# Kernel optimization log

Measured on AMD Instinct MI355X. Metric: run time of the kernel, lower is better.

Reference implementation:

```python
import jax, jax.numpy as jnp
import numpy as np

N = 100000   # KG_E: number of entities
D = 128      # hidden_dim == out_dim
H = 4        # n_heads
DH = D // H  # att_size
E = 1200000  # KG edges (avg degree 12)


def _layer_norm(x, g, b, eps=1e-5):
    mu = jnp.mean(x, -1, keepdims=True)
    var = jnp.mean((x - mu) ** 2, -1, keepdims=True)
    return (x - mu) * jax.lax.rsqrt(var + eps) * g + b


def setup_inputs() -> dict:
    key = jax.random.key(0)
    ks = jax.random.split(key, 16)
    p = lambda i, s: jax.random.normal(ks[i], s, jnp.float32) * 0.02
    loops = jnp.arange(N, dtype=jnp.int32)
    return {
        "ent_embed": jax.random.normal(ks[0], (N, D), jnp.float32),
        "edge_weight": jax.random.uniform(ks[1], (E,), jnp.float32),
        "ln1_g": jnp.ones(D, jnp.float32), "ln1_b": jnp.zeros(D, jnp.float32),
        "wq": p(2, (D, D)), "bq": jnp.zeros(D, jnp.float32),
        "wk": p(3, (D, D)), "bk": jnp.zeros(D, jnp.float32),
        "wv": p(4, (D, D)), "bv": jnp.zeros(D, jnp.float32),
        "wo": p(5, (D, D)), "bo": jnp.zeros(D, jnp.float32),
        "ln2_g": jnp.ones(D, jnp.float32), "ln2_b": jnp.zeros(D, jnp.float32),
        "w1": p(6, (D, D)), "b1": jnp.zeros(D, jnp.float32),  # ffn_size == hidden_dim here
        "w2": p(7, (D, D)), "b2": jnp.zeros(D, jnp.float32),
        "lmbda12": jnp.array([np.log10(6.0), 2.2 - np.log10(6.0)], jnp.float32),
        "gat_w": p(8, (D, D)), "gat_b": jnp.zeros(D, jnp.float32),
        "w_atten_r": p(9, (2 * D, 1)),
        "prelu_a": jnp.array(0.25, jnp.float32),
        "edge_index": jax.random.randint(ks[10], (2, E), 0, N, jnp.int32),
        "batch_ids": loops,
        # drop_neigh(drop_prob=0): batch COO edges + appended self-loops (node_num -> batch_ids)
        "batch_edge_index": jnp.concatenate(
            [jax.random.randint(ks[11], (2, E), 0, N, jnp.int32),
             jnp.stack([loops, loops])], axis=1),
    }


def _forward(ent_embed, edge_weight, ln1_g, ln1_b, wq, bq, wk, bk, wv, bv, wo, bo,
             ln2_g, ln2_b, w1, b1, w2, b2, lmbda12, gat_w, gat_b, w_atten_r, prelu_a,
             edge_index, batch_ids, batch_edge_index):
    # ---- pre-LN transformer encoder block; each entity is a length-1 sequence ----
    y = _layer_norm(ent_embed, ln1_g, ln1_b)
    q = (y @ wq + bq).reshape(N, H, DH)
    k = (y @ wk + bk).reshape(N, H, DH)
    v = (y @ wv + bv).reshape(N, H, DH)
    logits = jnp.sum(q * (DH ** -0.5) * k, -1, keepdims=True)  # [N,H,1]: single kv position
    attn = jax.nn.softmax(logits, axis=-1)                     # == 1.0 since seq_len == 1
    ctx = (attn * v).reshape(N, D)
    x = ent_embed + (ctx @ wo + bo)
    y = _layer_norm(x, ln2_g, ln2_b)
    gcn_in = x + (jax.nn.gelu(y @ w1 + b1, approximate=False) @ w2 + b2)

    # ---- GCN layer: lambda-weighted neighbor mean via sparse spmm ----
    row, col = edge_index[0], edge_index[1]
    neigh_sum = jax.ops.segment_sum(edge_weight[:, None] * gcn_in[col], row, num_segments=N)
    rowsum = jax.ops.segment_sum(edge_weight, row, num_segments=N)[:, None]
    l1, l2 = lmbda12[0], lmbda12[1]
    gcn_out = (gcn_in + l2 * neigh_sum) / (1.0 + l2 * rowsum) * l1

    # ---- GAT layer: gather -> per-edge attention -> scatter-normalize ----
    gat_in = gcn_out @ gat_w + gat_b
    brow, bcol = batch_edge_index[0], batch_edge_index[1]
    # cat([l, r]) @ w  ==  l @ w[:D] + r @ w[D:]  (avoids [E, 2D] intermediate)
    s_l = gat_in[batch_ids] @ w_atten_r[:D, 0]   # per left-slot node scalar
    s_r = gat_in @ w_atten_r[D:, 0]              # per node scalar
    e = s_l[brow] + s_r[bcol]
    att = jnp.exp(-jnp.where(e > 0, e, 0.2 * e))  # exp(-leaky_relu(e, 0.2))
    e_rowsum = jax.ops.segment_sum(att, brow, num_segments=N)[:, None]
    e_out = jax.ops.segment_sum(att[:, None] * gat_in[bcol], brow, num_segments=N)
    e_out = e_out * (1.0 / e_rowsum)
    return jnp.where(e_out > 0, e_out, prelu_a * e_out)  # PReLU


def reference(ent_embed, edge_weight, ln1_g, ln1_b, wq, bq, wk, bk, wv, bv, wo, bo,
              ln2_g, ln2_b, w1, b1, w2, b2, lmbda12, gat_w, gat_b, w_atten_r, prelu_a,
              edge_index, batch_ids, batch_edge_index):
    return _forward(ent_embed, edge_weight, ln1_g, ln1_b, wq, bq, wk, bk, wv, bv, wo, bo,
                    ln2_g, ln2_b, w1, b1, w2, b2, lmbda12, gat_w, gat_b, w_atten_r, prelu_a,
                    edge_index, batch_ids, batch_edge_index)
```

## Files before the change

### kernel.cpp

```cpp
#include <hip/hip_runtime.h>
#include <hip/hip_bf16.h>
#include <math.h>

#define D 128

typedef __attribute__((ext_vector_type(8))) short bf16x8_t;
typedef __attribute__((ext_vector_type(4))) float f32x4_t;

__device__ __forceinline__ unsigned short f2bf(float f){
    unsigned int x = __float_as_uint(f);
    unsigned int r = x + 0x7FFFu + ((x >> 16) & 1u);
    return (unsigned short)(r >> 16);
}

__device__ __forceinline__ float gelu_exact(float x){
    return 0.5f * x * (1.0f + erff(x * 0.70710678118654752f));
}


template<int R>
__device__ __forceinline__ void multiReduce(float* red, int j){
    __syncthreads();
    #pragma unroll
    for (int s = 64; s > 0; s >>= 1){
        if (j < s){
            #pragma unroll
            for (int r = 0; r < R; ++r) red[r*D + j] += red[r*D + j + s];
        }
        __syncthreads();
    }
}

template<int R>
__device__ __forceinline__ void matvec(const float* sh, const float* __restrict__ W,
                                       const float* __restrict__ bias, int j, float* acc){
    float bb = bias[j];
    #pragma unroll
    for (int r = 0; r < R; ++r) acc[r] = bb;
    #pragma unroll 8
    for (int i = 0; i < D; ++i){
        float w = W[i*D + j];
        #pragma unroll
        for (int r = 0; r < R; ++r) acc[r] += sh[r*D + i] * w;
    }
}

__global__ __launch_bounds__(256)
void k_cvt(const float* __restrict__ w0, const float* __restrict__ w1,
           const float* __restrict__ w2, const float* __restrict__ w3,
           unsigned short* __restrict__ out)
{
    int m = blockIdx.y;
    const float* W = (m == 0) ? w0 : (m == 1) ? w1 : (m == 2) ? w2 : w3;
    int o = blockIdx.x * 256 + threadIdx.x;
    int j  = o & 7;
    int l  = (o >> 3) & 63;
    int k0 = (o >> 9) & 3;
    int s  = o >> 11;
    int k  = 32*k0 + 8*(l >> 4) + j;
    int nn = 16*s + (l & 15);
    out[(size_t)m * 16384 + o] = f2bf(W[k*D + nn]);
}


__device__ __forceinline__ void mm_stage(const unsigned short* __restrict__ Wp,
                                         const float* __restrict__ bias,
                                         const unsigned short (*Xw)[136],
                                         int c, int g, int l, f32x4_t acc[8])
{
    #pragma unroll
    for (int s = 0; s < 8; ++s){
        float bb = bias[16*s + c];
        acc[s] = (f32x4_t){bb, bb, bb, bb};
    }
    #pragma unroll
    for (int k0 = 0; k0 < 4; ++k0){
        bf16x8_t a = *(const bf16x8_t*)&Xw[c][32*k0 + 8*g];
        #pragma unroll
        for (int s = 0; s < 8; ++s){
            bf16x8_t b = *(const bf16x8_t*)&Wp[(size_t)(((s*4 + k0)*64 + l) * 8)];
            acc[s] = __builtin_amdgcn_mfma_f32_16x16x32_bf16(a, b, acc[s], 0, 0, 0);
        }
    }
}

__global__ __launch_bounds__(256)
void k_dense(const float* __restrict__ ent,
             const float* __restrict__ g1, const float* __restrict__ be1,
             const float* __restrict__ g2, const float* __restrict__ be2,
             const float* __restrict__ bv, const float* __restrict__ bo,
             const float* __restrict__ b1, const float* __restrict__ b2,
             const unsigned short* __restrict__ Wp,
             float* __restrict__ gcn_in, int n)
{
    __shared__ unsigned short X[4][16][136];
    const int tid = threadIdx.x;
    const int wv_ = tid >> 6, l = tid & 63, c = l & 15, g = l >> 4;
    const int row0 = blockIdx.x * 64 + wv_ * 16;
    unsigned short (*Xw)[136] = X[wv_];

    float ev[8][4];
    #pragma unroll
    for (int s = 0; s < 8; ++s)
        #pragma unroll
        for (int r = 0; r < 4; ++r){
            int rr = row0 + 4*g + r; if (rr >= n) rr = n - 1;
            ev[s][r] = ent[(size_t)rr * D + 16*s + c];
        }

    {
        float gg[8], bb[8];
        #pragma unroll
        for (int s = 0; s < 8; ++s){ gg[s] = g1[16*s + c]; bb[s] = be1[16*s + c]; }
        #pragma unroll
        for (int r = 0; r < 4; ++r){
            float t = 0.0f;
            #pragma unroll
            for (int s = 0; s < 8; ++s) t += ev[s][r];
            t += __shfl_xor(t,1); t += __shfl_xor(t,2); t += __shfl_xor(t,4); t += __shfl_xor(t,8);
            float mu = t * (1.0f/128.0f);
            float q = 0.0f;
            #pragma unroll
            for (int s = 0; s < 8; ++s){ float d = ev[s][r]-mu; q += d*d; }
            q += __shfl_xor(q,1); q += __shfl_xor(q,2); q += __shfl_xor(q,4); q += __shfl_xor(q,8);
            float rs = rsqrtf(q*(1.0f/128.0f) + 1e-5f);
            #pragma unroll
            for (int s = 0; s < 8; ++s)
                Xw[4*g + r][16*s + c] = f2bf((ev[s][r]-mu)*rs*gg[s] + bb[s]);
        }
    }

    f32x4_t acc[8];

    mm_stage(Wp + 0*16384, bv, Xw, c, g, l, acc);
    #pragma unroll
    for (int s = 0; s < 8; ++s)
        #pragma unroll
        for (int r = 0; r < 4; ++r)
            Xw[4*g + r][16*s + c] = f2bf(acc[s][r]);

    mm_stage(Wp + 1*16384, bo, Xw, c, g, l, acc);
    #pragma unroll
    for (int s = 0; s < 8; ++s)
        #pragma unroll
        for (int r = 0; r < 4; ++r)
            ev[s][r] += acc[s][r];

    {
        float gg[8], bb[8];
        #pragma unroll
        for (int s = 0; s < 8; ++s){ gg[s] = g2[16*s + c]; bb[s] = be2[16*s + c]; }
        #pragma unroll
        for (int r = 0; r < 4; ++r){
            float t = 0.0f;
            #pragma unroll
            for (int s = 0; s < 8; ++s) t += ev[s][r];
            t += __shfl_xor(t,1); t += __shfl_xor(t,2); t += __shfl_xor(t,4); t += __shfl_xor(t,8);
            float mu = t * (1.0f/128.0f);
            float q = 0.0f;
            #pragma unroll
            for (int s = 0; s < 8; ++s){ float d = ev[s][r]-mu; q += d*d; }
            q += __shfl_xor(q,1); q += __shfl_xor(q,2); q += __shfl_xor(q,4); q += __shfl_xor(q,8);
            float rs = rsqrtf(q*(1.0f/128.0f) + 1e-5f);
            #pragma unroll
            for (int s = 0; s < 8; ++s)
                Xw[4*g + r][16*s + c] = f2bf((ev[s][r]-mu)*rs*gg[s] + bb[s]);
        }
    }

    mm_stage(Wp + 2*16384, b1, Xw, c, g, l, acc);
    #pragma unroll
    for (int s = 0; s < 8; ++s)
        #pragma unroll
        for (int r = 0; r < 4; ++r)
            Xw[4*g + r][16*s + c] = f2bf(gelu_exact(acc[s][r]));

    mm_stage(Wp + 3*16384, b2, Xw, c, g, l, acc);
    #pragma unroll
    for (int s = 0; s < 8; ++s)
        #pragma unroll
        for (int r = 0; r < 4; ++r){
            int rr = row0 + 4*g + r;
            if (rr < n) gcn_in[(size_t)rr * D + 16*s + c] = ev[s][r] + acc[s][r];
        }
}


__global__ __launch_bounds__(256)
void k_hist(const int* __restrict__ rows, int* __restrict__ deg, int E){
    int i = blockIdx.x * 256 + threadIdx.x;
    if (i < E) atomicAdd(&deg[rows[i]], 1);
}

__global__ __launch_bounds__(256)
void k_scan_partial(const int* __restrict__ deg, int* __restrict__ bsum, int n){
    __shared__ int s[256];
    int i = blockIdx.x * 256 + threadIdx.x;
    s[threadIdx.x] = (i < n) ? deg[i] : 0;
    __syncthreads();
    #pragma unroll
    for (int st = 128; st > 0; st >>= 1){
        if (threadIdx.x < st) s[threadIdx.x] += s[threadIdx.x + st];
        __syncthreads();
    }
    if (threadIdx.x == 0) bsum[blockIdx.x] = s[0];
}

__global__ __launch_bounds__(1024)
void k_scan_bsums(int* __restrict__ bsum, int nb){
    __shared__ int a[1024], b[1024];
    int t = threadIdx.x;
    int orig = (t < nb) ? bsum[t] : 0;
    int *src = a, *dst = b;
    src[t] = orig;
    __syncthreads();
    for (int off = 1; off < 1024; off <<= 1){
        dst[t] = src[t] + ((t >= off) ? src[t-off] : 0);
        __syncthreads();
        int* tmp = src; src = dst; dst = tmp;
    }
    if (t < nb) bsum[t] = src[t] - orig;
}

__global__ __launch_bounds__(256)
void k_scan_final(const int* __restrict__ deg, const int* __restrict__ bsum,
                  int* __restrict__ start, int* __restrict__ cur, int n, int total){
    __shared__ int a[256], b[256];
    int t = threadIdx.x;
    int i = blockIdx.x * 256 + t;
    int orig = (i < n) ? deg[i] : 0;
    int *src = a, *dst = b;
    src[t] = orig;
    __syncthreads();
    for (int off = 1; off < 256; off <<= 1){
        dst[t] = src[t] + ((t >= off) ? src[t-off] : 0);
        __syncthreads();
        int* tmp = src; src = dst; dst = tmp;
    }
    int excl = src[t] - orig + bsum[blockIdx.x];
    if (i < n){ start[i] = excl; cur[i] = excl; }
    if (i == n-1) start[n] = total;
}

__global__ __launch_bounds__(256)
void k_fill_gcn(const int* __restrict__ eidx, const float* __restrict__ ew,
                int* __restrict__ cur, int* __restrict__ colp, float* __restrict__ wp, int E){
    int i = blockIdx.x * 256 + threadIdx.x;
    if (i < E){
        int r = eidx[i];
        int pos = atomicAdd(&cur[r], 1);
        colp[pos] = eidx[E + i];
        wp[pos]   = ew[i];
    }
}

__global__ __launch_bounds__(256)
void k_fill_gat(const int* __restrict__ beidx, int* __restrict__ cur,
                int* __restrict__ colp, int E2){
    int i = blockIdx.x * 256 + threadIdx.x;
    if (i < E2){
        int r = beidx[i];
        int pos = atomicAdd(&cur[r], 1);
        colp[pos] = beidx[E2 + i];
    }
}

template<int R>
__global__ __launch_bounds__(128)
void k_gcn_pull_fin(const float* __restrict__ gcn_in,
                    const int* __restrict__ start, const int* __restrict__ colp,
                    const float* __restrict__ wp,
                    const float* __restrict__ lmbda,
                    const float* __restrict__ gat_w, const float* __restrict__ gat_b,
                    const float* __restrict__ watt,
                    float* __restrict__ gat_in,
                    float* __restrict__ dl, float* __restrict__ dr, int n)
{
    const int j = threadIdx.x;
    const int row0 = blockIdx.x * R;
    __shared__ float sh[R*D];
    __shared__ float red[R*D];
    float l1 = lmbda[0], l2 = lmbda[1];

    #pragma unroll
    for (int r = 0; r < R; ++r){
        int rr = row0 + r;
        if (rr < n){
            float acc = 0.0f, wsum = 0.0f;
            int s0 = start[rr], s1 = start[rr+1];
            for (int e = s0; e < s1; ++e){
                int   c = colp[e];
                float w = wp[e];
                acc  += w * gcn_in[(size_t)c * D + j];
                wsum += w;
            }
            float base = gcn_in[(size_t)rr * D + j];
            sh[r*D + j] = (base + l2 * acc) / (1.0f + l2 * wsum) * l1;
        } else {
            sh[r*D + j] = 0.0f;
        }
    }
    __syncthreads();

    float gv[R]; matvec<R>(sh, gat_w, gat_b, j, gv);
    #pragma unroll
    for (int r = 0; r < R; ++r){
        int rr = row0 + r;
        if (rr < n) gat_in[(size_t)rr * D + j] = gv[r];
    }

    float wl = watt[j], wr = watt[D + j];
    __syncthreads();
    #pragma unroll
    for (int r = 0; r < R; ++r) red[r*D + j] = gv[r] * wl;
    multiReduce<R>(red, j);
    if (j == 0){
        #pragma unroll
        for (int r = 0; r < R; ++r){ int rr = row0 + r; if (rr < n) dl[rr] = red[r*D]; }
    }
    __syncthreads();
    #pragma unroll
    for (int r = 0; r < R; ++r) red[r*D + j] = gv[r] * wr;
    multiReduce<R>(red, j);
    if (j == 0){
        #pragma unroll
        for (int r = 0; r < R; ++r){ int rr = row0 + r; if (rr < n) dr[rr] = red[r*D]; }
    }
}

template<int R>
__global__ __launch_bounds__(128)
void k_gat_out(const float* __restrict__ gat_in,
               const int* __restrict__ start2, const int* __restrict__ colp2,
               const int* __restrict__ bids,
               const float* __restrict__ dl, const float* __restrict__ dr,
               const float* __restrict__ prelu_a,
               float* __restrict__ out, int n)
{
    const int j = threadIdx.x;
    const int row0 = blockIdx.x * R;
    float pa = prelu_a[0];

    #pragma unroll
    for (int r = 0; r < R; ++r){
        int rr = row0 + r;
        if (rr < n){
            float dlv = dl[bids[rr]];
            int s0 = start2[rr], s1 = start2[rr+1];
            float acc = 0.0f, es = 0.0f;
            for (int e = s0; e < s1; ++e){
                int c = colp2[e];
                float ev = dlv + dr[c];
                float lr = ev > 0.0f ? ev : 0.2f * ev;
                float att = __expf(-lr);
                es  += att;
                acc += att * gat_in[(size_t)c * D + j];
            }
            float v = acc / es;
            out[(size_t)rr * D + j] = v > 0.0f ? v : pa * v;
        }
    }
}


extern "C" void kernel_launch(void* const* d_in, const int* in_sizes, int n_in,
                              void* d_out, int out_size, void* d_ws, size_t ws_size,
                              hipStream_t stream)
{
    const float* ent   = (const float*)d_in[0];
    const float* ew    = (const float*)d_in[1];
    const float* ln1_g = (const float*)d_in[2];
    const float* ln1_b = (const float*)d_in[3];
    const float* wv    = (const float*)d_in[8];
    const float* bv    = (const float*)d_in[9];
    const float* wo    = (const float*)d_in[10];
    const float* bo    = (const float*)d_in[11];
    const float* ln2_g = (const float*)d_in[12];
    const float* ln2_b = (const float*)d_in[13];
    const float* w1    = (const float*)d_in[14];
    const float* b1    = (const float*)d_in[15];
    const float* w2    = (const float*)d_in[16];
    const float* b2    = (const float*)d_in[17];
    const float* lmbda = (const float*)d_in[18];
    const float* gat_w = (const float*)d_in[19];
    const float* gat_b = (const float*)d_in[20];
    const float* watt  = (const float*)d_in[21];
    const float* prelu = (const float*)d_in[22];
    const int* eidx    = (const int*)d_in[23];
    const int* bids    = (const int*)d_in[24];
    const int* beidx   = (const int*)d_in[25];

    const int n  = in_sizes[24];
    const int E  = in_sizes[1];
    const int E2 = in_sizes[25] / 2;

    char* ws = (char*)d_ws;
    const size_t szND = (size_t)n * D * sizeof(float);
    size_t off = 0;
    float* bufA   = (float*)(ws + off); off += szND;
    float* bufB   = (float*)(ws + off); off += szND;
    float* dl     = (float*)(ws + off); off += (size_t)n * 4;
    float* dr     = (float*)(ws + off); off += (size_t)n * 4;
    int*   deg1   = (int*)(ws + off);   off += (size_t)n * 4;
    int*   deg2   = (int*)(ws + off);   off += (size_t)n * 4;
    int*   start1 = (int*)(ws + off);   off += (size_t)(n+1) * 4;
    int*   start2 = (int*)(ws + off);   off += (size_t)(n+1) * 4;
    int*   cur1   = (int*)(ws + off);   off += (size_t)n * 4;
    int*   cur2   = (int*)(ws + off);   off += (size_t)n * 4;
    int*   bsum   = (int*)(ws + off);   off += 1024 * 4;
    int*   colp1  = (int*)(ws + off);   off += (size_t)E * 4;
    float* wp1    = (float*)(ws + off); off += (size_t)E * 4;
    int*   colp2  = (int*)(ws + off);   off += (size_t)E2 * 4;
    off = (off + 15) & ~(size_t)15;
    unsigned short* Wp = (unsigned short*)(ws + off); off += (size_t)4 * 16384 * 2;

    constexpr int R = 4;
    const int nblk  = (n + R - 1) / R;
    const int nscan = (n + 255) / 256;

    k_cvt<<<dim3(64, 4), 256, 0, stream>>>(wv, wo, w1, w2, Wp);

    k_dense<<<(n + 63)/64, 256, 0, stream>>>(ent, ln1_g, ln1_b, ln2_g, ln2_b,
                                             bv, bo, b1, b2, Wp, bufA, n);

    hipMemsetAsync(deg1, 0, (size_t)2 * n * 4, stream);
    k_hist<<<(E + 255)/256, 256, 0, stream>>>(eidx, deg1, E);
    k_hist<<<(E2 + 255)/256, 256, 0, stream>>>(beidx, deg2, E2);

    k_scan_partial<<<nscan, 256, 0, stream>>>(deg1, bsum, n);
    k_scan_bsums<<<1, 1024, 0, stream>>>(bsum, nscan);
    k_scan_final<<<nscan, 256, 0, stream>>>(deg1, bsum, start1, cur1, n, E);
    k_fill_gcn<<<(E + 255)/256, 256, 0, stream>>>(eidx, ew, cur1, colp1, wp1, E);

    k_scan_partial<<<nscan, 256, 0, stream>>>(deg2, bsum, n);
    k_scan_bsums<<<1, 1024, 0, stream>>>(bsum, nscan);
    k_scan_final<<<nscan, 256, 0, stream>>>(deg2, bsum, start2, cur2, n, E2);
    k_fill_gat<<<(E2 + 255)/256, 256, 0, stream>>>(beidx, cur2, colp2, E2);

    k_gcn_pull_fin<R><<<nblk, 128, 0, stream>>>(bufA, start1, colp1, wp1, lmbda,
                                                gat_w, gat_b, watt, bufB, dl, dr, n);

    k_gat_out<R><<<nblk, 128, 0, stream>>>(bufB, start2, colp2, bids, dl, dr,
                                           prelu, (float*)d_out, n);
}
```

Baseline: 845.6 us.

## Fold GAT linear into dense kernel before aggregation; wave-per-row float2 pulls

The GAT projection (gat_w) is now applied per node inside the MFMA dense kernel, before the GCN neighbour aggregation. This relies on linearity: the weighted mean of projected rows equals the projection of the weighted mean, with the bias added afterwards. It removes the scalar fp32 matvec and the shared-memory reductions from the gather kernel. Both gather kernels now assign one wave per row, have each lane load float2, and compute dl/dr with wave shuffles. The cost is an extra bf16 rounding of the pre-projection activations, which can slightly change numerics.

Result: faster. 728.4 us (-13.9%).

```diff
diff --git a/kernel.cpp b/kernel.cpp
--- a/kernel.cpp
+++ b/kernel.cpp
@@ -17,41 +17,20 @@
     return 0.5f * x * (1.0f + erff(x * 0.70710678118654752f));
 }
 
-
-template<int R>
-__device__ __forceinline__ void multiReduce(float* red, int j){
-    __syncthreads();
-    #pragma unroll
-    for (int s = 64; s > 0; s >>= 1){
-        if (j < s){
-            #pragma unroll
-            for (int r = 0; r < R; ++r) red[r*D + j] += red[r*D + j + s];
-        }
-        __syncthreads();
-    }
-}
-
-template<int R>
-__device__ __forceinline__ void matvec(const float* sh, const float* __restrict__ W,
-                                       const float* __restrict__ bias, int j, float* acc){
-    float bb = bias[j];
-    #pragma unroll
-    for (int r = 0; r < R; ++r) acc[r] = bb;
-    #pragma unroll 8
-    for (int i = 0; i < D; ++i){
-        float w = W[i*D + j];
-        #pragma unroll
-        for (int r = 0; r < R; ++r) acc[r] += sh[r*D + i] * w;
-    }
+__device__ __forceinline__ float waveSum(float v){
+    #pragma unroll
+    for (int m = 1; m < 64; m <<= 1) v += __shfl_xor(v, m, 64);
+    return v;
 }
 
 __global__ __launch_bounds__(256)
 void k_cvt(const float* __restrict__ w0, const float* __restrict__ w1,
            const float* __restrict__ w2, const float* __restrict__ w3,
+           const float* __restrict__ w4,
            unsigned short* __restrict__ out)
 {
     int m = blockIdx.y;
-    const float* W = (m == 0) ? w0 : (m == 1) ? w1 : (m == 2) ? w2 : w3;
+    const float* W = (m == 0) ? w0 : (m == 1) ? w1 : (m == 2) ? w2 : (m == 3) ? w3 : w4;
     int o = blockIdx.x * 256 + threadIdx.x;
     int j  = o & 7;
     int l  = (o >> 3) & 63;
@@ -63,6 +42,7 @@
 }
 
 
+template<bool HASB>
 __device__ __forceinline__ void mm_stage(const unsigned short* __restrict__ Wp,
                                          const float* __restrict__ bias,
                                          const unsigned short (*Xw)[136],
@@ -70,7 +50,7 @@
 {
     #pragma unroll
     for (int s = 0; s < 8; ++s){
-        float bb = bias[16*s + c];
+        float bb = HASB ? bias[16*s + c] : 0.0f;
         acc[s] = (f32x4_t){bb, bb, bb, bb};
     }
     #pragma unroll
@@ -91,7 +71,7 @@
              const float* __restrict__ bv, const float* __restrict__ bo,
              const float* __restrict__ b1, const float* __restrict__ b2,
              const unsigned short* __restrict__ Wp,
-             float* __restrict__ gcn_in, int n)
+             float* __restrict__ Zout, int n)
 {
     __shared__ unsigned short X[4][16][136];
     const int tid = threadIdx.x;
@@ -132,14 +112,14 @@
 
     f32x4_t acc[8];
 
-    mm_stage(Wp + 0*16384, bv, Xw, c, g, l, acc);
+    mm_stage<true>(Wp + 0*16384, bv, Xw, c, g, l, acc);
     #pragma unroll
     for (int s = 0; s < 8; ++s)
         #pragma unroll
         for (int r = 0; r < 4; ++r)
             Xw[4*g + r][16*s + c] = f2bf(acc[s][r]);
 
-    mm_stage(Wp + 1*16384, bo, Xw, c, g, l, acc);
+    mm_stage<true>(Wp + 1*16384, bo, Xw, c, g, l, acc);
     #pragma unroll
     for (int s = 0; s < 8; ++s)
         #pragma unroll
@@ -168,20 +148,27 @@
         }
     }
 
-    mm_stage(Wp + 2*16384, b1, Xw, c, g, l, acc);
+    mm_stage<true>(Wp + 2*16384, b1, Xw, c, g, l, acc);
     #pragma unroll
     for (int s = 0; s < 8; ++s)
         #pragma unroll
         for (int r = 0; r < 4; ++r)
             Xw[4*g + r][16*s + c] = f2bf(gelu_exact(acc[s][r]));
 
-    mm_stage(Wp + 3*16384, b2, Xw, c, g, l, acc);
+    mm_stage<true>(Wp + 3*16384, b2, Xw, c, g, l, acc);
+    #pragma unroll
+    for (int s = 0; s < 8; ++s)
+        #pragma unroll
+        for (int r = 0; r < 4; ++r)
+            Xw[4*g + r][16*s + c] = f2bf(ev[s][r] + acc[s][r]);
+
+    mm_stage<false>(Wp + 4*16384, nullptr, Xw, c, g, l, acc);
     #pragma unroll
     for (int s = 0; s < 8; ++s)
         #pragma unroll
         for (int r = 0; r < 4; ++r){
             int rr = row0 + 4*g + r;
-            if (rr < n) gcn_in[(size_t)rr * D + 16*s + c] = ev[s][r] + acc[s][r];
+            if (rr < n) Zout[(size_t)rr * D + 16*s + c] = acc[s][r];
         }
 }
 
@@ -265,71 +252,52 @@
     }
 }
 
-template<int R>
-__global__ __launch_bounds__(128)
-void k_gcn_pull_fin(const float* __restrict__ gcn_in,
-                    const int* __restrict__ start, const int* __restrict__ colp,
-                    const float* __restrict__ wp,
-                    const float* __restrict__ lmbda,
-                    const float* __restrict__ gat_w, const float* __restrict__ gat_b,
-                    const float* __restrict__ watt,
-                    float* __restrict__ gat_in,
-                    float* __restrict__ dl, float* __restrict__ dr, int n)
-{
-    const int j = threadIdx.x;
-    const int row0 = blockIdx.x * R;
-    __shared__ float sh[R*D];
-    __shared__ float red[R*D];
-    float l1 = lmbda[0], l2 = lmbda[1];
-
-    #pragma unroll
-    for (int r = 0; r < R; ++r){
+#define PW 4
+__global__ __launch_bounds__(256)
+void k_gcn_pull(const float* __restrict__ Z,
+                const int* __restrict__ start, const int* __restrict__ colp,
+                const float* __restrict__ wp,
+                const float* __restrict__ lmbda,
+                const float* __restrict__ gat_b, const float* __restrict__ watt,
+                float* __restrict__ gat_in,
+                float* __restrict__ dl, float* __restrict__ dr, int n)
+{
+    const int l   = threadIdx.x & 63;
+    const int wv_ = threadIdx.x >> 6;
+    const int c0  = 2*l;
+    const float l1 = lmbda[0], l2 = lmbda[1];
+    const float2 gb = *(const float2*)&gat_b[c0];
+    const float2 wl = *(const float2*)&watt[c0];
+    const float2 wr = *(const float2*)&watt[D + c0];
+    const int row0 = (blockIdx.x * 4 + wv_) * PW;
+
+    #pragma unroll
+    for (int r = 0; r < PW; ++r){
         int rr = row0 + r;
         if (rr < n){
-            float acc = 0.0f, wsum = 0.0f;
-            int s0 = start[rr], s1 = start[rr+1];
+            int rs = __builtin_amdgcn_readfirstlane(rr);
+            int s0 = start[rs], s1 = start[rs+1];
+            float2 base = *(const float2*)&Z[(size_t)rs * D + c0];
+            float accx = 0.0f, accy = 0.0f, wsum = 0.0f;
             for (int e = s0; e < s1; ++e){
                 int   c = colp[e];
                 float w = wp[e];
-                acc  += w * gcn_in[(size_t)c * D + j];
-                wsum += w;
+                float2 zr = *(const float2*)&Z[(size_t)c * D + c0];
+                accx += w * zr.x; accy += w * zr.y; wsum += w;
             }
-            float base = gcn_in[(size_t)rr * D + j];
-            sh[r*D + j] = (base + l2 * acc) / (1.0f + l2 * wsum) * l1;
-        } else {
-            sh[r*D + j] = 0.0f;
-        }
-    }
-    __syncthreads();
-
-    float gv[R]; matvec<R>(sh, gat_w, gat_b, j, gv);
-    #pragma unroll
-    for (int r = 0; r < R; ++r){
-        int rr = row0 + r;
-        if (rr < n) gat_in[(size_t)rr * D + j] = gv[r];
-    }
-
-    float wl = watt[j], wr = watt[D + j];
-    __syncthreads();
-    #pragma unroll
-    for (int r = 0; r < R; ++r) red[r*D + j] = gv[r] * wl;
-    multiReduce<R>(red, j);
-    if (j == 0){
-        #pragma unroll
-        for (int r = 0; r < R; ++r){ int rr = row0 + r; if (rr < n) dl[rr] = red[r*D]; }
-    }
-    __syncthreads();
-    #pragma unroll
-    for (int r = 0; r < R; ++r) red[r*D + j] = gv[r] * wr;
-    multiReduce<R>(red, j);
-    if (j == 0){
-        #pragma unroll
-        for (int r = 0; r < R; ++r){ int rr = row0 + r; if (rr < n) dr[rr] = red[r*D]; }
-    }
-}
-
-template<int R>
-__global__ __launch_bounds__(128)
+            float inv = l1 / (1.0f + l2 * wsum);
+            float gx = (base.x + l2*accx) * inv + gb.x;
+            float gy = (base.y + l2*accy) * inv + gb.y;
+            float2 o; o.x = gx; o.y = gy;
+            *(float2*)&gat_in[(size_t)rs * D + c0] = o;
+            float dlv = waveSum(gx*wl.x + gy*wl.y);
+            float drv = waveSum(gx*wr.x + gy*wr.y);
+            if (l == 0){ dl[rs] = dlv; dr[rs] = drv; }
+        }
+    }
+}
+
+__global__ __launch_bounds__(256)
 void k_gat_out(const float* __restrict__ gat_in,
                const int* __restrict__ start2, const int* __restrict__ colp2,
                const int* __restrict__ bids,
@@ -337,27 +305,34 @@
                const float* __restrict__ prelu_a,
                float* __restrict__ out, int n)
 {
-    const int j = threadIdx.x;
-    const int row0 = blockIdx.x * R;
-    float pa = prelu_a[0];
-
-    #pragma unroll
-    for (int r = 0; r < R; ++r){
+    const int l   = threadIdx.x & 63;
+    const int wv_ = threadIdx.x >> 6;
+    const int c0  = 2*l;
+    const float pa = prelu_a[0];
+    const int row0 = (blockIdx.x * 4 + wv_) * PW;
+
+    #pragma unroll
+    for (int r = 0; r < PW; ++r){
         int rr = row0 + r;
         if (rr < n){
-            float dlv = dl[bids[rr]];
-            int s0 = start2[rr], s1 = start2[rr+1];
-            float acc = 0.0f, es = 0.0f;
+            int rs = __builtin_amdgcn_readfirstlane(rr);
+            float dlv = dl[bids[rs]];
+            int s0 = start2[rs], s1 = start2[rs+1];
+            float accx = 0.0f, accy = 0.0f, es = 0.0f;
             for (int e = s0; e < s1; ++e){
                 int c = colp2[e];
                 float ev = dlv + dr[c];
                 float lr = ev > 0.0f ? ev : 0.2f * ev;
                 float att = __expf(-lr);
-                es  += att;
-                acc += att * gat_in[(size_t)c * D + j];
+                float2 g = *(const float2*)&gat_in[(size_t)c * D + c0];
+                accx += att * g.x; accy += att * g.y; es += att;
             }
-            float v = acc / es;
-            out[(size_t)rr * D + j] = v > 0.0f ? v : pa * v;
+            float is = 1.0f / es;
+            float vx = accx * is, vy = accy * is;
+            float2 o;
+            o.x = vx > 0.0f ? vx : pa * vx;
+            o.y = vy > 0.0f ? vy : pa * vy;
+            *(float2*)&out[(size_t)rr * D + c0] = o;
         }
     }
 }
@@ -412,13 +387,12 @@
     float* wp1    = (float*)(ws + off); off += (size_t)E * 4;
     int*   colp2  = (int*)(ws + off);   off += (size_t)E2 * 4;
     off = (off + 15) & ~(size_t)15;
-    unsigned short* Wp = (unsigned short*)(ws + off); off += (size_t)4 * 16384 * 2;
-
-    constexpr int R = 4;
-    const int nblk  = (n + R - 1) / R;
+    unsigned short* Wp = (unsigned short*)(ws + off); off += (size_t)5 * 16384 * 2;
+
     const int nscan = (n + 255) / 256;
-
-    k_cvt<<<dim3(64, 4), 256, 0, stream>>>(wv, wo, w1, w2, Wp);
+    const int npull = (n + 4*PW - 1) / (4*PW);
+
+    k_cvt<<<dim3(64, 5), 256, 0, stream>>>(wv, wo, w1, w2, gat_w, Wp);
 
     k_dense<<<(n + 63)/64, 256, 0, stream>>>(ent, ln1_g, ln1_b, ln2_g, ln2_b,
                                              bv, bo, b1, b2, Wp, bufA, n);
@@ -437,9 +411,9 @@
     k_scan_final<<<nscan, 256, 0, stream>>>(deg2, bsum, start2, cur2, n, E2);
     k_fill_gat<<<(E2 + 255)/256, 256, 0, stream>>>(beidx, cur2, colp2, E2);
 
-    k_gcn_pull_fin<R><<<nblk, 128, 0, stream>>>(bufA, start1, colp1, wp1, lmbda,
-                                                gat_w, gat_b, watt, bufB, dl, dr, n);
-
-    k_gat_out<R><<<nblk, 128, 0, stream>>>(bufB, start2, colp2, bids, dl, dr,
-                                           prelu, (float*)d_out, n);
-}
+    k_gcn_pull<<<npull, 256, 0, stream>>>(bufA, start1, colp1, wp1, lmbda,
+                                          gat_b, watt, bufB, dl, dr, n);
+
+    k_gat_out<<<npull, 256, 0, stream>>>(bufB, start2, colp2, bids, dl, dr,
+                                         prelu, (float*)d_out, n);
+}
```
